# Kernel tuning notes

Hardware: AMD Instinct MI355X
Metric: run time of the kernel (lower is better)

## Reference

```python
import jax, jax.numpy as jnp
import numpy as np
import math

D_MODEL = 1024
N_HEADS = 16
HEAD_DIM = D_MODEL // N_HEADS
FEAT = 16
WINDOW = 64
EPS_NORM = 1e-6
EPS_LIN = 1e-6
CHUNK = 128


def setup_inputs() -> dict:
    key = jax.random.key(0)
    ks = jax.random.split(key, 7)
    B, T = 2, 2048
    s = 0.02
    return {
        'x': jax.random.normal(ks[0], (B, T, D_MODEL), jnp.float32),
        'norm_w': jnp.ones((D_MODEL,), jnp.float32),
        'Wq': jax.random.normal(ks[1], (D_MODEL, D_MODEL), jnp.float32) * s,
        'Wk': jax.random.normal(ks[2], (D_MODEL, D_MODEL), jnp.float32) * s,
        'Wv': jax.random.normal(ks[3], (D_MODEL, D_MODEL), jnp.float32) * s,
        'Wqf': jax.random.normal(ks[4], (HEAD_DIM, FEAT), jnp.float32) * s,
        'Wkf': jax.random.normal(ks[5], (HEAD_DIM, FEAT), jnp.float32) * s,
        'Wout': jax.random.normal(ks[6], (2 * D_MODEL, D_MODEL), jnp.float32) * s,
    }


def rmsnorm(x, w):
    return x * jax.lax.rsqrt(jnp.mean(x * x, axis=-1, keepdims=True) + EPS_NORM) * w


def taylor_feature_map(x):
    # phi(x) = [1, x, x_i*x_j * (0.5 if i==j else 1/sqrt(2)) for i<=j]
    d = x.shape[-1]
    iu, ju = jnp.triu_indices(d)  # row-major (i, j>=i) matches torch loop order
    scale = jnp.where(iu == ju, 0.5, 1.0 / math.sqrt(2.0)).astype(x.dtype)
    quad = x[..., iu] * x[..., ju] * scale
    ones = jnp.ones(x.shape[:-1] + (1,), dtype=x.dtype)
    return jnp.concatenate([ones, x, quad], axis=-1)  # (..., 1+d+d(d+1)/2)


def linear_attention_causal(q_phi, k_phi, v):
    # Chunked-parallel causal linear attention: y_t = q_t @ KV_t / (q_t @ Ksum_t + eps)
    B, T, H, F = q_phi.shape
    D = v.shape[-1]
    Nc = T // CHUNK
    qc = q_phi.reshape(B, Nc, CHUNK, H, F).transpose(1, 0, 2, 3, 4)  # (Nc,B,C,H,F)
    kc = k_phi.reshape(B, Nc, CHUNK, H, F).transpose(1, 0, 2, 3, 4)
    vc = v.reshape(B, Nc, CHUNK, H, D).transpose(1, 0, 2, 3, 4)      # (Nc,B,C,H,D)
    causal = jnp.tril(jnp.ones((CHUNK, CHUNK), dtype=q_phi.dtype))   # include diagonal

    def step(carry, inp):
        kv, ksum = carry                      # (B,H,F,D), (B,H,F)
        qb, kb, vb = inp
        A = jnp.einsum('bchf,bshf->bhcs', qb, kb) * causal  # intra-chunk quadratic scores
        y = jnp.einsum('bhcs,bshd->bchd', A, vb) + jnp.einsum('bchf,bhfd->bchd', qb, kv)
        z = jnp.einsum('bhcs->bch', A) + jnp.einsum('bchf,bhf->bch', qb, ksum)
        kv = kv + jnp.einsum('bshf,bshd->bhfd', kb, vb)
        ksum = ksum + kb.sum(axis=1)
        return (kv, ksum), y / (z[..., None] + EPS_LIN)

    kv0 = jnp.zeros((B, H, F, D), dtype=q_phi.dtype)
    ks0 = jnp.zeros((B, H, F), dtype=q_phi.dtype)
    _, ys = jax.lax.scan(step, (kv0, ks0), (qc, kc, vc))
    return ys.transpose(1, 0, 2, 3, 4).reshape(B, T, H, D)


def sliding_window_attention(q, k, v):
    B, T, H, D = q.shape
    scale = 1.0 / math.sqrt(D)
    t = jnp.arange(T)
    allowed = (t[None, :] <= t[:, None]) & (t[None, :] >= t[:, None] - WINDOW)  # (T,T)
    scores = jnp.einsum('bqhd,bkhd->bhqk', q, k) * scale
    scores = jnp.where(allowed[None, None], scores, -jnp.inf)
    attn = jax.nn.softmax(scores, axis=-1)
    out = jnp.einsum('bhqk,bkhd->bqhd', attn, v)
    return out.reshape(B, T, H * D)


def reference(x, norm_w, Wq, Wk, Wv, Wqf, Wkf, Wout):
    B, T, _ = x.shape
    h = rmsnorm(x, norm_w)
    q = (h @ Wq).reshape(B, T, N_HEADS, HEAD_DIM)
    k = (h @ Wk).reshape(B, T, N_HEADS, HEAD_DIM)
    v = (h @ Wv).reshape(B, T, N_HEADS, HEAD_DIM)
    q_phi = taylor_feature_map(q @ Wqf)
    k_phi = taylor_feature_map(k @ Wkf)
    lin = linear_attention_causal(q_phi, k_phi, v).reshape(B, T, D_MODEL)
    win = sliding_window_attention(q, k, v)
    out = jnp.concatenate([lin, win], axis=-1) @ Wout
    return x + out
```

## Files before the change

### kernel.cpp

```cpp
#include <hip/hip_runtime.h>
#include <math.h>

#define BB 2
#define TT 2048
#define DM 1024
#define NH 16
#define HD 64
#define FEAT 16
#define WIN 64
#define RTOT (BB*TT)

typedef __bf16 bf16x8 __attribute__((ext_vector_type(8)));
typedef float  f32x4  __attribute__((ext_vector_type(4)));

__device__ __forceinline__ unsigned short f2bf(float f) {
    union { float f; unsigned u; } v; v.f = f;
    unsigned r = v.u + 0x7FFFu + ((v.u >> 16) & 1u);
    return (unsigned short)(r >> 16);
}
__device__ __forceinline__ float bf2f(unsigned short u) {
    union { unsigned u; float f; } v; v.u = ((unsigned)u) << 16; return v.f;
}

__device__ __forceinline__ void gl2lds16(const void* g, void* l) {
    __builtin_amdgcn_global_load_lds(
        (const __attribute__((address_space(1))) void*)g,
        (__attribute__((address_space(3))) void*)l, 16, 0, 0);
}

__global__ __launch_bounds__(256) void rmsnorm_kernel(const float* __restrict__ x,
                                                      const float* __restrict__ w,
                                                      unsigned short* __restrict__ h_bf) {
    int row = blockIdx.x;
    int tid = threadIdx.x;
    const float4* xr = (const float4*)(x + (size_t)row * DM);
    float4 xv = xr[tid];
    float ss = xv.x*xv.x + xv.y*xv.y + xv.z*xv.z + xv.w*xv.w;
    #pragma unroll
    for (int off = 32; off > 0; off >>= 1) ss += __shfl_down(ss, off, 64);
    __shared__ float red[4];
    if ((tid & 63) == 0) red[tid >> 6] = ss;
    __syncthreads();
    float tot = red[0] + red[1] + red[2] + red[3];
    float scale = rsqrtf(tot * (1.0f / DM) + 1e-6f);
    float4 wv = ((const float4*)w)[tid];
    ushort4 o;
    o.x = f2bf(xv.x * scale * wv.x);
    o.y = f2bf(xv.y * scale * wv.y);
    o.z = f2bf(xv.z * scale * wv.z);
    o.w = f2bf(xv.w * scale * wv.w);
    *(ushort4*)&h_bf[(size_t)row * DM + tid * 4] = o;
}

__global__ __launch_bounds__(256) void transpose_bf16_kernel(const float* __restrict__ W0,
                                                             const float* __restrict__ W1,
                                                             const float* __restrict__ W2,
                                                             const float* __restrict__ W3,
                                                             unsigned short* __restrict__ T0,
                                                             unsigned short* __restrict__ T1,
                                                             unsigned short* __restrict__ T2,
                                                             unsigned short* __restrict__ T3) {
    int z = blockIdx.z;
    int K = (z == 3) ? 2048 : 1024;
    const int N = 1024;
    if (blockIdx.y * 64 >= K) return;
    const float* W = (z == 0) ? W0 : (z == 1) ? W1 : (z == 2) ? W2 : W3;
    unsigned short* WT = (z == 0) ? T0 : (z == 1) ? T1 : (z == 2) ? T2 : T3;
    __shared__ float tile[64][65];
    int k0 = blockIdx.y * 64, n0 = blockIdx.x * 64;
    int t = threadIdx.x;
    int r = t >> 4, c4 = (t & 15) * 4;
    #pragma unroll
    for (int i = 0; i < 4; i++) {
        float4 vv = *(const float4*)&W[(size_t)(k0 + r + i*16) * N + n0 + c4];
        tile[r + i*16][c4 + 0] = vv.x;
        tile[r + i*16][c4 + 1] = vv.y;
        tile[r + i*16][c4 + 2] = vv.z;
        tile[r + i*16][c4 + 3] = vv.w;
    }
    __syncthreads();
    int rn = t >> 2, kq = (t & 3) * 16;
    unsigned short u[16];
    #pragma unroll
    for (int i = 0; i < 16; i++) u[i] = f2bf(tile[kq + i][rn]);
    size_t base = (size_t)(n0 + rn) * K + k0 + kq;
    *(uint4*)&WT[base]     = *(uint4*)&u[0];
    *(uint4*)&WT[base + 8] = *(uint4*)&u[8];
}

template<int LD, int KITERS>
__device__ __forceinline__ void gemm256_core(const unsigned short* __restrict__ A,
                                             const unsigned short* __restrict__ BT,
                                             unsigned short* __restrict__ Cb,
                                             int k0g) {
    const int N = 1024;
    __shared__ __align__(16) unsigned short As[3 * 256 * 32];
    __shared__ __align__(16) unsigned short Bs[3 * 256 * 32];
    int tid = threadIdx.x;
    int lane = tid & 63;
    int w = tid >> 6;
    int wm = (w >> 2) * 128, wn = (w & 3) * 64;
    int m0 = blockIdx.y * 256, n0 = blockIdx.x * 256;
    int hi = lane >> 4;
    int l15 = lane & 15;

    int c0 = tid, c1 = tid + 512;
    int r0 = c0 >> 2, kh0 = ((c0 & 3) - (r0 >> 1)) & 3;
    int r1 = c1 >> 2, kh1 = ((c1 & 3) - (r1 >> 1)) & 3;
    const unsigned short* aP0 = A  + (size_t)(m0 + r0) * LD + k0g + kh0 * 8;
    const unsigned short* aP1 = A  + (size_t)(m0 + r1) * LD + k0g + kh1 * 8;
    const unsigned short* bP0 = BT + (size_t)(n0 + r0) * LD + k0g + kh0 * 8;
    const unsigned short* bP1 = BT + (size_t)(n0 + r1) * LD + k0g + kh1 * 8;
    unsigned short* asD0 = &As[c0 * 8];
    unsigned short* asD1 = &As[c1 * 8];
    unsigned short* bsD0 = &Bs[c0 * 8];
    unsigned short* bsD1 = &Bs[c1 * 8];

    int aOff[8], bOff[4];
    #pragma unroll
    for (int i = 0; i < 8; i++) {
        int m = wm + i * 16 + l15;
        aOff[i] = m * 32 + (((hi + (m >> 1)) & 3) * 8);
    }
    #pragma unroll
    for (int j = 0; j < 4; j++) {
        int n = wn + j * 16 + l15;
        bOff[j] = n * 32 + (((hi + (n >> 1)) & 3) * 8);
    }

    f32x4 acc[8][4];
    #pragma unroll
    for (int i = 0; i < 8; i++)
        #pragma unroll
        for (int j = 0; j < 4; j++)
            acc[i][j] = (f32x4){0.f, 0.f, 0.f, 0.f};

#define STAGE256(ts, bf) do {                                   \
        int _o = (ts) * 32;                                     \
        int _b = (bf) * 8192;                                   \
        gl2lds16(aP0 + _o, asD0 + _b);                          \
        gl2lds16(aP1 + _o, asD1 + _b);                          \
        gl2lds16(bP0 + _o, bsD0 + _b);                          \
        gl2lds16(bP1 + _o, bsD1 + _b);                          \
    } while (0)

    STAGE256(0, 0);
    STAGE256(1, 1);

    for (int t = 0; t < KITERS; t++) {
        int rd = t % 3;
        if (t + 1 < KITERS) {
            asm volatile("s_waitcnt vmcnt(4)" ::: "memory");
        } else {
            asm volatile("s_waitcnt vmcnt(0)" ::: "memory");
        }
        __builtin_amdgcn_s_barrier();
        asm volatile("" ::: "memory");
        if (t + 2 < KITERS) STAGE256(t + 2, (t + 2) % 3);
        const unsigned short* Ab = &As[rd * 8192];
        const unsigned short* Bb = &Bs[rd * 8192];
        bf16x8 af[8], bfr[4];
        #pragma unroll
        for (int i = 0; i < 8; i++) af[i] = *(const bf16x8*)&Ab[aOff[i]];
        #pragma unroll
        for (int j = 0; j < 4; j++) bfr[j] = *(const bf16x8*)&Bb[bOff[j]];
        __builtin_amdgcn_s_setprio(1);
        #pragma unroll
        for (int i = 0; i < 8; i++)
            #pragma unroll
            for (int j = 0; j < 4; j++)
                acc[i][j] = __builtin_amdgcn_mfma_f32_16x16x32_bf16(af[i], bfr[j], acc[i][j], 0, 0, 0);
        __builtin_amdgcn_s_setprio(0);
    }
#undef STAGE256

    #pragma unroll
    for (int i = 0; i < 8; i++) {
        #pragma unroll
        for (int j = 0; j < 4; j++) {
            int col = n0 + wn + j * 16 + l15;
            #pragma unroll
            for (int r = 0; r < 4; r++) {
                int row = m0 + wm + i * 16 + hi * 4 + r;
                Cb[(size_t)row * N + col] = f2bf(acc[i][j][r]);
            }
        }
    }
}

__global__ __launch_bounds__(512, 2) void gemm_qkv_mfma(const unsigned short* __restrict__ A,
                                                        const unsigned short* __restrict__ BT0,
                                                        const unsigned short* __restrict__ BT1,
                                                        const unsigned short* __restrict__ BT2,
                                                        unsigned short* __restrict__ C0,
                                                        unsigned short* __restrict__ C1,
                                                        unsigned short* __restrict__ C2) {
    const unsigned short* BT = (blockIdx.z == 0) ? BT0 : (blockIdx.z == 1) ? BT1 : BT2;
    unsigned short* C = (blockIdx.z == 0) ? C0 : (blockIdx.z == 1) ? C1 : C2;
    gemm256_core<1024, 32>(A, BT, C, 0);
}

__global__ __launch_bounds__(512, 2) void gemm_out_mfma(const unsigned short* __restrict__ A,
                                                        const unsigned short* __restrict__ BT,
                                                        unsigned short* __restrict__ P0,
                                                        unsigned short* __restrict__ P1,
                                                        unsigned short* __restrict__ P2,
                                                        unsigned short* __restrict__ P3) {
    unsigned short* P = (blockIdx.z == 0) ? P0 : (blockIdx.z == 1) ? P1
                      : (blockIdx.z == 2) ? P2 : P3;
    gemm256_core<2048, 16>(A, BT, P, blockIdx.z * 512);
}

__global__ __launch_bounds__(256) void out_reduce_kernel(const float* __restrict__ x,
                                                         const unsigned short* __restrict__ P0,
                                                         const unsigned short* __restrict__ P1,
                                                         const unsigned short* __restrict__ P2,
                                                         const unsigned short* __restrict__ P3,
                                                         float* __restrict__ out) {
    int g = blockIdx.x * 256 + threadIdx.x;
    size_t e = (size_t)g * 4;
    float4 xv = *(const float4*)&x[e];
    ushort4 a = *(const ushort4*)&P0[e];
    ushort4 b = *(const ushort4*)&P1[e];
    ushort4 c = *(const ushort4*)&P2[e];
    ushort4 d = *(const ushort4*)&P3[e];
    float4 o;
    o.x = xv.x + bf2f(a.x) + bf2f(b.x) + bf2f(c.x) + bf2f(d.x);
    o.y = xv.y + bf2f(a.y) + bf2f(b.y) + bf2f(c.y) + bf2f(d.y);
    o.z = xv.z + bf2f(a.z) + bf2f(b.z) + bf2f(c.z) + bf2f(d.z);
    o.w = xv.w + bf2f(a.w) + bf2f(b.w) + bf2f(c.w) + bf2f(d.w);
    *(float4*)&out[e] = o;
}

__global__ __launch_bounds__(256) void feat_kernel(const unsigned short* __restrict__ qb,
                                                   const unsigned short* __restrict__ kb,
                                                   const float* __restrict__ Wqf,
                                                   const float* __restrict__ Wkf,
                                                   unsigned short* __restrict__ qf,
                                                   unsigned short* __restrict__ kf) {
    __shared__ float Wl[HD * FEAT];
    const unsigned short* src = blockIdx.z ? kb : qb;
    const float* Wm = blockIdx.z ? Wkf : Wqf;
    unsigned short* dst = blockIdx.z ? kf : qf;
    int tid = threadIdx.x;
    ((float4*)Wl)[tid] = ((const float4*)Wm)[tid];
    __syncthreads();
    int gid = blockIdx.x * 256 + tid;
    int f = gid & 15;
    int rowh = gid >> 4;
    const unsigned short* s = src + (size_t)rowh * HD;
    float acc = 0.f;
    #pragma unroll
    for (int d = 0; d < HD; d++) acc += bf2f(s[d]) * Wl[d * FEAT + f];
    dst[gid] = f2bf(acc);
}

__global__ __launch_bounds__(256) void win_mfma_kernel(const unsigned short* __restrict__ q_bf,
                                                       const unsigned short* __restrict__ k_bf,
                                                       const unsigned short* __restrict__ v_bf,
                                                       unsigned short* __restrict__ cat_bf) {
    int qtile = blockIdx.x;
    int bh = blockIdx.y;
    int h = bh & 15;
    int b = bh >> 4;
    int tid = threadIdx.x;
    int lane = tid & 63;
    int wv = tid >> 6;
    int qr0 = wv * 16;
    int t0 = qtile * 64;
    int k0 = t0 - 64;

    __shared__ __align__(16) unsigned short Qs[64 * 64];
    __shared__ __align__(16) unsigned short Ks[128 * 64];
    __shared__ __align__(16) unsigned short Vt[64 * 128];
    __shared__ __align__(16) unsigned short Pl[64 * 128];

    #pragma unroll
    for (int half = 0; half < 2; half++) {
        int slot = tid + half * 256;
        int row = slot >> 3, pos = slot & 7;
        int o = (pos - row) & 7;
        gl2lds16(q_bf + (size_t)(b * TT + t0 + row) * (NH * HD) + h * HD + o * 8,
                 &Qs[slot * 8]);
    }
    #pragma unroll
    for (int qd = 0; qd < 4; qd++) {
        int slot = tid + qd * 256;
        int row = slot >> 3, pos = slot & 7;
        int o = (pos - row) & 7;
        int kg = k0 + row;
        if (kg >= 0) {
            gl2lds16(k_bf + (size_t)(b * TT + kg) * (NH * HD) + h * HD + o * 8,
                     &Ks[slot * 8]);
        } else {
            uint4 z = {0, 0, 0, 0};
            *(uint4*)&Ks[slot * 8] = z;
        }
    }
    {
        int kk = tid & 127;
        int dh = tid >> 7;
        int kg = k0 + kk;
        unsigned short tmp[32];
        if (kg >= 0) {
            size_t base = (size_t)(b * TT + kg) * (NH * HD) + h * HD + dh * 32;
            *(uint4*)&tmp[0]  = *(const uint4*)&v_bf[base];
            *(uint4*)&tmp[8]  = *(const uint4*)&v_bf[base + 8];
            *(uint4*)&tmp[16] = *(const uint4*)&v_bf[base + 16];
            *(uint4*)&tmp[24] = *(const uint4*)&v_bf[base + 24];
        } else {
            #pragma unroll
            for (int d = 0; d < 32; d++) tmp[d] = 0;
        }
        int o = kk >> 3, klow = kk & 7;
        #pragma unroll
        for (int d = 0; d < 32; d++) {
            int dim = dh * 32 + d;
            Vt[dim * 128 + ((o + dim) & 15) * 8 + klow] = tmp[d];
        }
    }
    __syncthreads();

    int hi = lane >> 4;
    int lan15 = lane & 15;
    f32x4 sc[8];
    #pragma unroll
    for (int nt = 0; nt < 8; nt++) sc[nt] = (f32x4){0.f, 0.f, 0.f, 0.f};
    #pragma unroll
    for (int ks = 0; ks < 2; ks++) {
        int m = qr0 + lan15;
        int oA = ks * 4 + hi;
        bf16x8 a = *(const bf16x8*)&Qs[m * 64 + ((oA + m) & 7) * 8];
        #pragma unroll
        for (int nt = 0; nt < 8; nt++) {
            int n = nt * 16 + lan15;
            bf16x8 bb = *(const bf16x8*)&Ks[n * 64 + ((oA + n) & 7) * 8];
            sc[nt] = __builtin_amdgcn_mfma_f32_16x16x32_bf16(a, bb, sc[nt], 0, 0, 0);
        }
    }

    float lrow[4];
    #pragma unroll
    for (int r = 0; r < 4; r++) {
        int tq = t0 + qr0 + hi * 4 + r;
        float mx = -1e30f;
        #pragma unroll
        for (int nt = 0; nt < 8; nt++) {
            int s = k0 + nt * 16 + lan15;
            bool ok = (s >= 0) && (s <= tq) && (s >= tq - WIN);
            float vv = ok ? sc[nt][r] * 0.125f : -1e30f;
            sc[nt][r] = vv;
            mx = fmaxf(mx, vv);
        }
        #pragma unroll
        for (int off = 1; off < 16; off <<= 1) mx = fmaxf(mx, __shfl_xor(mx, off, 64));
        float ls = 0.f;
        #pragma unroll
        for (int nt = 0; nt < 8; nt++) {
            float e = __expf(sc[nt][r] - mx);
            sc[nt][r] = e;
            ls += e;
        }
        #pragma unroll
        for (int off = 1; off < 16; off <<= 1) ls += __shfl_xor(ls, off, 64);
        lrow[r] = ls;
    }

    #pragma unroll
    for (int nt = 0; nt < 8; nt++) {
        #pragma unroll
        for (int r = 0; r < 4; r++) {
            int row = qr0 + hi * 4 + r;
            int col = nt * 16 + lan15;
            Pl[row * 128 + (((col >> 3) + row) & 15) * 8 + (col & 7)] = f2bf(sc[nt][r]);
        }
    }
    __syncthreads();

    f32x4 y[4];
    #pragma unroll
    for (int nt = 0; nt < 4; nt++) y[nt] = (f32x4){0.f, 0.f, 0.f, 0.f};
    #pragma unroll
    for (int ks = 0; ks < 4; ks++) {
        int m = qr0 + lan15;
        int oA = ks * 4 + hi;
        bf16x8 a = *(const bf16x8*)&Pl[m * 128 + ((oA + m) & 15) * 8];
        #pragma unroll
        for (int nt = 0; nt < 4; nt++) {
            int n = nt * 16 + lan15;
            bf16x8 bb = *(const bf16x8*)&Vt[n * 128 + ((oA + n) & 15) * 8];
            y[nt] = __builtin_amdgcn_mfma_f32_16x16x32_bf16(a, bb, y[nt], 0, 0, 0);
        }
    }

    #pragma unroll
    for (int nt = 0; nt < 4; nt++) {
        #pragma unroll
        for (int r = 0; r < 4; r++) {
            int row = qr0 + hi * 4 + r;
            int dim = nt * 16 + lan15;
            cat_bf[(size_t)(b * TT + t0 + row) * (2 * DM) + DM + h * HD + dim] =
                f2bf(y[nt][r] / lrow[r]);
        }
    }
}

#define PHI 160
#define NCH 32
#define KVROWS 65
#define CH_STRIDE ((size_t)32 * KVROWS * PHI)

__global__ __launch_bounds__(256) void lin_kv_kernel(const unsigned short* __restrict__ kf,
                                                     const unsigned short* __restrict__ v_bf,
                                                     unsigned short* __restrict__ kvbuf) {
    int c = blockIdx.x, bh = blockIdx.y;
    int h = bh & 15, b = bh >> 4;
    int tid = threadIdx.x, lane = tid & 63, w = tid >> 6;
    int hi = lane >> 4, l15 = lane & 15;

    __shared__ unsigned short kf_l[64 * 16];
    __shared__ __align__(16) unsigned short PhiT[192 * 76];
    __shared__ __align__(16) unsigned short Vt[80 * 64];
    __shared__ unsigned short iu[136], ju[136];
    __shared__ float sclut[136];

    if (tid < 136) {
        int qq = tid, i = 0;
        while (qq >= 16 - i) { qq -= 16 - i; i++; }
        iu[tid] = (unsigned short)i; ju[tid] = (unsigned short)(i + qq);
        sclut[tid] = (qq == 0) ? 0.5f : 0.70710678118654752f;
    }
    {
        int r = tid >> 2, f4 = (tid & 3) * 4;
        *(ushort4*)&kf_l[r * 16 + f4] =
            *(const ushort4*)&kf[((size_t)((b * TT + c * 64 + r) * NH + h)) * FEAT + f4];
    }
    {
        int p = tid & 31, dq = (tid >> 5) * 8;
        size_t base0 = ((size_t)(b * TT + c * 64 + 2 * p)) * DM + h * HD + dq;
        unsigned short a[8], bq[8];
        *(uint4*)a  = *(const uint4*)&v_bf[base0];
        *(uint4*)bq = *(const uint4*)&v_bf[base0 + DM];
        int colo = p >> 2, coll = (2 * p) & 7;
        #pragma unroll
        for (int d = 0; d < 8; d++) {
            int row = dq + d;
            ushort2 u; u.x = a[d]; u.y = bq[d];
            *(ushort2*)&Vt[row * 64 + ((colo + row) & 7) * 8 + coll] = u;
        }
        #pragma unroll
        for (int i = 0; i < 4; i++) {
            int e = tid + i * 256;
            Vt[(64 + (e >> 6)) * 64 + (e & 63)] = 0x3F80;
        }
    }
    __syncthreads();
    {
        int s = tid & 63, fb = tid >> 6;
        const unsigned short* krow = &kf_l[s * 16];
        for (int it = 0; it < 40; it++) {
            int f = fb * 40 + it;
            float val;
            if (f == 0) val = 1.f;
            else if (f < 17) val = bf2f(krow[f - 1]);
            else if (f < 153) { int qq = f - 17; val = bf2f(krow[iu[qq]]) * bf2f(krow[ju[qq]]) * sclut[qq]; }
            else val = 0.f;
            PhiT[f * 76 + s] = f2bf(val);
        }
    }
    __syncthreads();
    f32x4 acc[5][3];
    #pragma unroll
    for (int m = 0; m < 5; m++)
        #pragma unroll
        for (int j = 0; j < 3; j++) acc[m][j] = (f32x4){0.f, 0.f, 0.f, 0.f};
    #pragma unroll
    for (int ks = 0; ks < 2; ks++) {
        bf16x8 bfrag[3];
        #pragma unroll
        for (int j = 0; j < 3; j++)
            bfrag[j] = *(const bf16x8*)&PhiT[((3 * w + j) * 16 + l15) * 76 + ks * 32 + hi * 8];
        #pragma unroll
        for (int m = 0; m < 5; m++) {
            int mrow = m * 16 + l15;
            bf16x8 afrag = *(const bf16x8*)&Vt[mrow * 64 + (((ks * 4 + hi) + mrow) & 7) * 8];
            #pragma unroll
            for (int j = 0; j < 3; j++)
                acc[m][j] = __builtin_amdgcn_mfma_f32_16x16x32_bf16(afrag, bfrag[j], acc[m][j], 0, 0, 0);
        }
    }
    size_t obase = ((size_t)c * 32 + bh) * (KVROWS * PHI);
    #pragma unroll
    for (int m = 0; m < 5; m++) {
        #pragma unroll
        for (int j = 0; j < 3; j++) {
            int f = (3 * w + j) * 16 + l15;
            if (f >= PHI) continue;
            #pragma unroll
            for (int r = 0; r < 4; r++) {
                int row = m * 16 + hi * 4 + r;
                if (row >= KVROWS) continue;
                kvbuf[obase + row * PHI + f] = f2bf(acc[m][j][r]);
            }
        }
    }
}

__global__ __launch_bounds__(256) void lin_scan_kernel(unsigned short* __restrict__ kvbuf) {
    int e = blockIdx.x * 256 + threadIdx.x;
    int bh = blockIdx.y;
    if (e >= KVROWS * PHI) return;
    float acc = 0.f;
    size_t off = (size_t)bh * (KVROWS * PHI) + e;
    for (int c = 0; c < NCH; c++) {
        float vv = bf2f(kvbuf[off]);
        kvbuf[off] = f2bf(acc);
        acc += vv;
        off += CH_STRIDE;
    }
}

__global__ __launch_bounds__(256) void lin_out_kernel(const unsigned short* __restrict__ qf,
                                                      const unsigned short* __restrict__ kf,
                                                      const unsigned short* __restrict__ v_bf,
                                                      const unsigned short* __restrict__ kvbuf,
                                                      unsigned short* __restrict__ cat_bf) {
    int c = blockIdx.x, bh = blockIdx.y;
    int h = bh & 15, b = bh >> 4;
    int tid = threadIdx.x, lane = tid & 63, w = tid >> 6;
    int hi = lane >> 4, l15 = lane & 15;

    __shared__ unsigned short qf_l[64 * 16];
    __shared__ __align__(16) unsigned short kf_lb[64 * 34];
    __shared__ __align__(16) unsigned short KVS_l[80 * 164];
    __shared__ __align__(16) unsigned short Vt[80 * 64];
    __shared__ __align__(16) unsigned short Phi_l[64 * 164];
    __shared__ __align__(16) unsigned short P_l[64 * 64];
    __shared__ unsigned short iu[136], ju[136];
    __shared__ float sclut[136];

    if (tid < 136) {
        int qq = tid, i = 0;
        while (qq >= 16 - i) { qq -= 16 - i; i++; }
        iu[tid] = (unsigned short)i; ju[tid] = (unsigned short)(i + qq);
        sclut[tid] = (qq == 0) ? 0.5f : 0.70710678118654752f;
    }
    {
        int r = tid >> 2, f4 = (tid & 3) * 4;
        *(ushort4*)&qf_l[r * 16 + f4] =
            *(const ushort4*)&qf[((size_t)((b * TT + c * 64 + r) * NH + h)) * FEAT + f4];
    }
    {
        int r = tid >> 2, f4 = (tid & 3) * 4;
        *(ushort4*)&kf_lb[r * 34 + f4] =
            *(const ushort4*)&kf[((size_t)((b * TT + c * 64 + r) * NH + h)) * FEAT + f4];
        ushort4 z4 = {0, 0, 0, 0};
        *(ushort4*)&kf_lb[r * 34 + 16 + f4] = z4;
    }
    {
        int p = tid & 31, dq = (tid >> 5) * 8;
        size_t base0 = ((size_t)(b * TT + c * 64 + 2 * p)) * DM + h * HD + dq;
        unsigned short a[8], bq[8];
        *(uint4*)a  = *(const uint4*)&v_bf[base0];
        *(uint4*)bq = *(const uint4*)&v_bf[base0 + DM];
        int colo = p >> 2, coll = (2 * p) & 7;
        #pragma unroll
        for (int d = 0; d < 8; d++) {
            int row = dq + d;
            ushort2 u; u.x = a[d]; u.y = bq[d];
            *(ushort2*)&Vt[row * 64 + ((colo + row) & 7) * 8 + coll] = u;
        }
        #pragma unroll
        for (int i = 0; i < 4; i++) {
            int e = tid + i * 256;
            Vt[(64 + (e >> 6)) * 64 + (e & 63)] = 0x3F80;
        }
    }
    {
        size_t gbase = ((size_t)c * 32 + bh) * (KVROWS * PHI);
        #pragma unroll
        for (int i = 0; i < 11; i++) {
            int e4 = tid + i * 256;
            if (e4 < KVROWS * 40) {
                int r = e4 / 40, q4 = (e4 % 40) * 4;
                *(ushort4*)&KVS_l[r * 164 + q4] =
                    *(const ushort4*)&kvbuf[gbase + r * PHI + q4];
            }
        }
        #pragma unroll
        for (int i = 0; i < 3; i++) {
            int e4 = tid + i * 256;
            if (e4 < 15 * 40) {
                int r = 65 + e4 / 40, q4 = (e4 % 40) * 4;
                ushort4 z4 = {0, 0, 0, 0};
                *(ushort4*)&KVS_l[r * 164 + q4] = z4;
            }
        }
    }
    __syncthreads();

    {
        int s = tid & 63, fb = tid >> 6;
        const unsigned short* qrow = &qf_l[s * 16];
        for (int it = 0; it < 40; it++) {
            int f = fb * 40 + it;
            float val;
            if (f == 0) val = 1.f;
            else if (f < 17) val = bf2f(qrow[f - 1]);
            else if (f < 153) { int qq = f - 17; val = bf2f(qrow[iu[qq]]) * bf2f(qrow[ju[qq]]) * sclut[qq]; }
            else val = 0.f;
            Phi_l[s * 164 + f] = f2bf(val);
        }
    }
    __syncthreads();

    f32x4 acc[5];
    #pragma unroll
    for (int n = 0; n < 5; n++) acc[n] = (f32x4){0.f, 0.f, 0.f, 0.f};

    int t_m = w * 16 + l15;

    #pragma unroll
    for (int ks = 0; ks < 5; ks++) {
        bf16x8 af = *(const bf16x8*)&Phi_l[t_m * 164 + ks * 32 + hi * 8];
        #pragma unroll
        for (int n = 0; n < 5; n++) {
            bf16x8 bb = *(const bf16x8*)&KVS_l[(n * 16 + l15) * 164 + ks * 32 + hi * 8];
            acc[n] = __builtin_amdgcn_mfma_f32_16x16x32_bf16(af, bb, acc[n], 0, 0, 0);
        }
    }

    {
        union { unsigned short u[8]; bf16x8 v; } aq;
        #pragma unroll
        for (int j = 0; j < 8; j++) {
            int f = hi * 8 + j;
            aq.u[j] = (f < 16) ? qf_l[t_m * 16 + f] : (unsigned short)0;
        }
        #pragma unroll
        for (int n = 0; n < 4; n++) {
            bf16x8 bk = *(const bf16x8*)&kf_lb[(n * 16 + l15) * 34 + hi * 8];
            f32x4 zv = {0.f, 0.f, 0.f, 0.f};
            f32x4 sc = __builtin_amdgcn_mfma_f32_16x16x32_bf16(aq.v, bk, zv, 0, 0, 0);
            int sl = n * 16 + l15;
            #pragma unroll
            for (int r = 0; r < 4; r++) {
                int rl = w * 16 + hi * 4 + r;
                float sv = 1.f + 0.5f * sc[r];
                sv = sv * sv;
                if (sl > rl) sv = 0.f;
                P_l[rl * 64 + (((sl >> 3) + rl) & 7) * 8 + (sl & 7)] = f2bf(sv);
            }
        }
    }
    __syncthreads();

    #pragma unroll
    for (int ks = 0; ks < 2; ks++) {
        int oA = ks * 4 + hi;
        bf16x8 a = *(const bf16x8*)&P_l[t_m * 64 + ((oA + t_m) & 7) * 8];
        #pragma unroll
        for (int n = 0; n < 5; n++) {
            int nrow = n * 16 + l15;
            bf16x8 bb = *(const bf16x8*)&Vt[nrow * 64 + ((oA + nrow) & 7) * 8];
            acc[n] = __builtin_amdgcn_mfma_f32_16x16x32_bf16(a, bb, acc[n], 0, 0, 0);
        }
    }

    #pragma unroll
    for (int r = 0; r < 4; r++) {
        float zz = __shfl(acc[4][r], (lane & 48), 64);
        int token = c * 64 + w * 16 + hi * 4 + r;
        #pragma unroll
        for (int n = 0; n < 4; n++) {
            int d = n * 16 + l15;
            cat_bf[((size_t)(b * TT + token)) * (2 * DM) + h * HD + d] =
                f2bf(acc[n][r] / (zz + 1e-6f));
        }
    }
}

extern "C" void kernel_launch(void* const* d_in, const int* in_sizes, int n_in,
                              void* d_out, int out_size, void* d_ws, size_t ws_size,
                              hipStream_t stream) {
    const float* x      = (const float*)d_in[0];
    const float* norm_w = (const float*)d_in[1];
    const float* Wq     = (const float*)d_in[2];
    const float* Wk     = (const float*)d_in[3];
    const float* Wv     = (const float*)d_in[4];
    const float* Wqf    = (const float*)d_in[5];
    const float* Wkf    = (const float*)d_in[6];
    const float* Wout   = (const float*)d_in[7];
    float* out = (float*)d_out;

    char* p = (char*)d_ws;
    unsigned short* h_bf = (unsigned short*)p; p += (size_t)RTOT * DM * 2;
    unsigned short* WqT  = (unsigned short*)p; p += (size_t)DM * DM * 2;
    unsigned short* WkT  = (unsigned short*)p; p += (size_t)DM * DM * 2;
    unsigned short* WvT  = (unsigned short*)p; p += (size_t)DM * DM * 2;
    unsigned short* WoT  = (unsigned short*)p; p += (size_t)DM * 2 * DM * 2;
    unsigned short* q_bf = (unsigned short*)p; p += (size_t)RTOT * DM * 2;
    unsigned short* k_bf = (unsigned short*)p; p += (size_t)RTOT * DM * 2;
    unsigned short* v_bf = (unsigned short*)p; p += (size_t)RTOT * DM * 2;
    unsigned short* qf_bf = (unsigned short*)p; p += (size_t)RTOT * NH * FEAT * 2;
    unsigned short* kf_bf = (unsigned short*)p; p += (size_t)RTOT * NH * FEAT * 2;
    unsigned short* cat_bf = (unsigned short*)p; p += (size_t)RTOT * 2 * DM * 2;
    unsigned short* kvbuf  = (unsigned short*)p; p += (size_t)NCH * 32 * KVROWS * PHI * 2;
    unsigned short* P0 = (unsigned short*)p; p += (size_t)RTOT * DM * 2;
    unsigned short* P1 = (unsigned short*)p; p += (size_t)RTOT * DM * 2;
    unsigned short* P2 = h_bf;
    unsigned short* P3 = q_bf;

    rmsnorm_kernel<<<RTOT, 256, 0, stream>>>(x, norm_w, h_bf);
    transpose_bf16_kernel<<<dim3(16, 32, 4), 256, 0, stream>>>(Wq, Wk, Wv, Wout, WqT, WkT, WvT, WoT);
    gemm_qkv_mfma<<<dim3(4, 16, 3), 512, 0, stream>>>(h_bf, WqT, WkT, WvT, q_bf, k_bf, v_bf);
    feat_kernel<<<dim3((RTOT * NH * FEAT) / 256, 1, 2), 256, 0, stream>>>(q_bf, k_bf, Wqf, Wkf, qf_bf, kf_bf);
    win_mfma_kernel<<<dim3(TT / 64, BB * NH), 256, 0, stream>>>(q_bf, k_bf, v_bf, cat_bf);
    lin_kv_kernel<<<dim3(NCH, BB * NH), 256, 0, stream>>>(kf_bf, v_bf, kvbuf);
    lin_scan_kernel<<<dim3((KVROWS * PHI + 255) / 256, BB * NH), 256, 0, stream>>>(kvbuf);
    lin_out_kernel<<<dim3(NCH, BB * NH), 256, 0, stream>>>(qf_bf, kf_bf, v_bf, kvbuf, cat_bf);
    gemm_out_mfma<<<dim3(4, 16, 4), 512, 0, stream>>>(cat_bf, WoT, P0, P1, P2, P3);
    out_reduce_kernel<<<RTOT * DM / 1024, 256, 0, stream>>>(x, P0, P1, P2, P3, out);
}
```

Measured before the change: 268.4 us.

## Restructure bf16 GEMM mainloop into 8-phase ping-pong schedule with K=64 tiles

Replaces the triple-buffered K=32 mainloop with a double-buffered K=64 tile split into four LDS regions (A/B for two K-halves). Each iteration is broken into four phases that interleave LDS fragment reads, async global-to-LDS staging of the next tile, barriers, and MFMA bursts, so memory traffic overlaps compute at finer grain. It adds many extra barriers per iteration and keeps roughly the same LDS footprint, which could cost synchronization overhead or occupancy.

```diff
diff --git a/kernel.cpp b/kernel.cpp
--- a/kernel.cpp
+++ b/kernel.cpp
@@ -88,14 +88,13 @@
     *(uint4*)&WT[base + 8] = *(uint4*)&u[8];
 }
 
-template<int LD, int KITERS>
-__device__ __forceinline__ void gemm256_core(const unsigned short* __restrict__ A,
-                                             const unsigned short* __restrict__ BT,
-                                             unsigned short* __restrict__ Cb,
-                                             int k0g) {
+template<int LD, int NT>
+__device__ __forceinline__ void gemm8p_core(const unsigned short* __restrict__ A,
+                                            const unsigned short* __restrict__ BT,
+                                            unsigned short* __restrict__ Cb,
+                                            int k0g) {
     const int N = 1024;
-    __shared__ __align__(16) unsigned short As[3 * 256 * 32];
-    __shared__ __align__(16) unsigned short Bs[3 * 256 * 32];
+    __shared__ __align__(16) unsigned short L[2][4][256 * 32];
     int tid = threadIdx.x;
     int lane = tid & 63;
     int w = tid >> 6;
@@ -107,25 +106,21 @@
     int c0 = tid, c1 = tid + 512;
     int r0 = c0 >> 2, kh0 = ((c0 & 3) - (r0 >> 1)) & 3;
     int r1 = c1 >> 2, kh1 = ((c1 & 3) - (r1 >> 1)) & 3;
-    const unsigned short* aP0 = A  + (size_t)(m0 + r0) * LD + k0g + kh0 * 8;
-    const unsigned short* aP1 = A  + (size_t)(m0 + r1) * LD + k0g + kh1 * 8;
-    const unsigned short* bP0 = BT + (size_t)(n0 + r0) * LD + k0g + kh0 * 8;
-    const unsigned short* bP1 = BT + (size_t)(n0 + r1) * LD + k0g + kh1 * 8;
-    unsigned short* asD0 = &As[c0 * 8];
-    unsigned short* asD1 = &As[c1 * 8];
-    unsigned short* bsD0 = &Bs[c0 * 8];
-    unsigned short* bsD1 = &Bs[c1 * 8];
-
-    int aOff[8], bOff[4];
+    const unsigned short* aS0 = A  + (size_t)(m0 + r0) * LD + k0g + kh0 * 8;
+    const unsigned short* aS1 = A  + (size_t)(m0 + r1) * LD + k0g + kh1 * 8;
+    const unsigned short* bS0 = BT + (size_t)(n0 + r0) * LD + k0g + kh0 * 8;
+    const unsigned short* bS1 = BT + (size_t)(n0 + r1) * LD + k0g + kh1 * 8;
+
+    int aoff[8], boff[4];
     #pragma unroll
     for (int i = 0; i < 8; i++) {
         int m = wm + i * 16 + l15;
-        aOff[i] = m * 32 + (((hi + (m >> 1)) & 3) * 8);
+        aoff[i] = m * 32 + (((hi + (m >> 1)) & 3) * 8);
     }
     #pragma unroll
     for (int j = 0; j < 4; j++) {
         int n = wn + j * 16 + l15;
-        bOff[j] = n * 32 + (((hi + (n >> 1)) & 3) * 8);
+        boff[j] = n * 32 + (((hi + (n >> 1)) & 3) * 8);
     }
 
     f32x4 acc[8][4];
@@ -135,44 +130,93 @@
         for (int j = 0; j < 4; j++)
             acc[i][j] = (f32x4){0.f, 0.f, 0.f, 0.f};
 
-#define STAGE256(ts, bf) do {                                   \
-        int _o = (ts) * 32;                                     \
-        int _b = (bf) * 8192;                                   \
-        gl2lds16(aP0 + _o, asD0 + _b);                          \
-        gl2lds16(aP1 + _o, asD1 + _b);                          \
-        gl2lds16(bP0 + _o, bsD0 + _b);                          \
-        gl2lds16(bP1 + _o, bsD1 + _b);                          \
+#define STG8(kt, bf, rg) do {                                         \
+        int _go = (kt) * 64 + ((rg) >> 1) * 32;                       \
+        unsigned short* _d = &L[bf][rg][0];                           \
+        if ((rg) & 1) { gl2lds16(bS0 + _go, _d + c0 * 8);             \
+                        gl2lds16(bS1 + _go, _d + c1 * 8); }           \
+        else          { gl2lds16(aS0 + _go, _d + c0 * 8);             \
+                        gl2lds16(aS1 + _go, _d + c1 * 8); }           \
     } while (0)
 
-    STAGE256(0, 0);
-    STAGE256(1, 1);
-
-    for (int t = 0; t < KITERS; t++) {
-        int rd = t % 3;
-        if (t + 1 < KITERS) {
+    STG8(0, 0, 0); STG8(0, 0, 1); STG8(0, 0, 2); STG8(0, 0, 3);
+    asm volatile("s_waitcnt vmcnt(4)" ::: "memory");
+    __builtin_amdgcn_s_barrier();
+
+    for (int t = 0; t < NT; t++) {
+        int rd = t & 1, st = rd ^ 1;
+        bool stg = (t + 1 < NT);
+        const unsigned short* A0 = &L[rd][0][0];
+        const unsigned short* B0 = &L[rd][1][0];
+        const unsigned short* A1 = &L[rd][2][0];
+        const unsigned short* B1 = &L[rd][3][0];
+        bf16x8 af[4], bfr[4];
+
+        #pragma unroll
+        for (int i = 0; i < 4; i++) af[i] = *(const bf16x8*)&A0[aoff[i]];
+        #pragma unroll
+        for (int j = 0; j < 4; j++) bfr[j] = *(const bf16x8*)&B0[boff[j]];
+        if (stg) STG8(t + 1, st, 0);
+        __builtin_amdgcn_s_barrier();
+        __builtin_amdgcn_s_setprio(1);
+        #pragma unroll
+        for (int i = 0; i < 4; i++)
+            #pragma unroll
+            for (int j = 0; j < 4; j++)
+                acc[i][j] = __builtin_amdgcn_mfma_f32_16x16x32_bf16(af[i], bfr[j], acc[i][j], 0, 0, 0);
+        __builtin_amdgcn_s_setprio(0);
+        __builtin_amdgcn_s_barrier();
+
+        #pragma unroll
+        for (int i = 0; i < 4; i++) af[i] = *(const bf16x8*)&A0[aoff[4 + i]];
+        if (stg) {
+            STG8(t + 1, st, 1);
             asm volatile("s_waitcnt vmcnt(4)" ::: "memory");
         } else {
             asm volatile("s_waitcnt vmcnt(0)" ::: "memory");
         }
         __builtin_amdgcn_s_barrier();
-        asm volatile("" ::: "memory");
-        if (t + 2 < KITERS) STAGE256(t + 2, (t + 2) % 3);
-        const unsigned short* Ab = &As[rd * 8192];
-        const unsigned short* Bb = &Bs[rd * 8192];
-        bf16x8 af[8], bfr[4];
-        #pragma unroll
-        for (int i = 0; i < 8; i++) af[i] = *(const bf16x8*)&Ab[aOff[i]];
-        #pragma unroll
-        for (int j = 0; j < 4; j++) bfr[j] = *(const bf16x8*)&Bb[bOff[j]];
         __builtin_amdgcn_s_setprio(1);
         #pragma unroll
-        for (int i = 0; i < 8; i++)
+        for (int i = 0; i < 4; i++)
+            #pragma unroll
+            for (int j = 0; j < 4; j++)
+                acc[4 + i][j] = __builtin_amdgcn_mfma_f32_16x16x32_bf16(af[i], bfr[j], acc[4 + i][j], 0, 0, 0);
+        __builtin_amdgcn_s_setprio(0);
+        __builtin_amdgcn_s_barrier();
+
+        #pragma unroll
+        for (int i = 0; i < 4; i++) af[i] = *(const bf16x8*)&A1[aoff[i]];
+        #pragma unroll
+        for (int j = 0; j < 4; j++) bfr[j] = *(const bf16x8*)&B1[boff[j]];
+        if (stg) STG8(t + 1, st, 2);
+        __builtin_amdgcn_s_barrier();
+        __builtin_amdgcn_s_setprio(1);
+        #pragma unroll
+        for (int i = 0; i < 4; i++)
             #pragma unroll
             for (int j = 0; j < 4; j++)
                 acc[i][j] = __builtin_amdgcn_mfma_f32_16x16x32_bf16(af[i], bfr[j], acc[i][j], 0, 0, 0);
         __builtin_amdgcn_s_setprio(0);
-    }
-#undef STAGE256
+        __builtin_amdgcn_s_barrier();
+
+        #pragma unroll
+        for (int i = 0; i < 4; i++) af[i] = *(const bf16x8*)&A1[aoff[4 + i]];
+        if (stg) {
+            STG8(t + 1, st, 3);
+            asm volatile("s_waitcnt vmcnt(4)" ::: "memory");
+        }
+        __builtin_amdgcn_s_barrier();
+        __builtin_amdgcn_s_setprio(1);
+        #pragma unroll
+        for (int i = 0; i < 4; i++)
+            #pragma unroll
+            for (int j = 0; j < 4; j++)
+                acc[4 + i][j] = __builtin_amdgcn_mfma_f32_16x16x32_bf16(af[i], bfr[j], acc[4 + i][j], 0, 0, 0);
+        __builtin_amdgcn_s_setprio(0);
+        __builtin_amdgcn_s_barrier();
+    }
+#undef STG8
 
     #pragma unroll
     for (int i = 0; i < 8; i++) {
@@ -197,7 +241,7 @@
                                                         unsigned short* __restrict__ C2) {
     const unsigned short* BT = (blockIdx.z == 0) ? BT0 : (blockIdx.z == 1) ? BT1 : BT2;
     unsigned short* C = (blockIdx.z == 0) ? C0 : (blockIdx.z == 1) ? C1 : C2;
-    gemm256_core<1024, 32>(A, BT, C, 0);
+    gemm8p_core<1024, 16>(A, BT, C, 0);
 }
 
 __global__ __launch_bounds__(512, 2) void gemm_out_mfma(const unsigned short* __restrict__ A,
@@ -208,7 +252,7 @@
                                                         unsigned short* __restrict__ P3) {
     unsigned short* P = (blockIdx.z == 0) ? P0 : (blockIdx.z == 1) ? P1
                       : (blockIdx.z == 2) ? P2 : P3;
-    gemm256_core<2048, 16>(A, BT, P, blockIdx.z * 512);
+    gemm8p_core<2048, 8>(A, BT, P, blockIdx.z * 512);
 }
 
 __global__ __launch_bounds__(256) void out_reduce_kernel(const float* __restrict__ x,
```

Result: faster. 254.1 us (-5.3%).
